# Kernel tuning notes

Measured on AMD Instinct MI355X. Metric: run time of the kernel, lower is better.

Reference implementation:

```python
import jax, jax.numpy as jnp
import numpy as np
import math

K_L = 16
EPS = 1e-5


def _knn_idx(xyt, k):
    # xyt: [B,N,3] -> idx of k nearest (incl. self), ascending distance. [B,N,k]
    sq = jnp.sum(xyt * xyt, axis=-1)                      # [B,N]
    d2 = sq[:, :, None] + sq[:, None, :] - 2.0 * jnp.einsum('bnd,bmd->bnm', xyt, xyt)
    _, idx = jax.lax.top_k(-d2, k)                        # smallest distances first
    return idx


def _gather(x, idx):
    # x: [B,N,D], idx: [B,N,K] -> [B,N,K,D]
    return jax.vmap(lambda p, i: p[i])(x, idx)


def setup_inputs() -> dict:
    key = jax.random.key(0)
    ks = jax.random.split(key, 6)
    B, N, C_in, C = 4, 8192, 64, 64
    xytp = jax.random.normal(ks[0], (B, N, 4), jnp.float32)
    features = jax.random.normal(ks[1], (B, N, C_in), jnp.float32)
    pe_w1 = jax.random.normal(ks[2], (4, C), jnp.float32) * (1.0 / math.sqrt(4))
    pe_b1 = jnp.zeros((C,), jnp.float32)
    pe_w2 = jax.random.normal(ks[3], (C, C), jnp.float32) * (1.0 / math.sqrt(C))
    pe_b2 = jnp.zeros((C,), jnp.float32)
    lt_w = jax.random.normal(ks[4], (C_in, 3 * C), jnp.float32) * (1.0 / math.sqrt(C_in))
    lt_b = jnp.zeros((3 * C,), jnp.float32)
    ln_g = jnp.ones((C,), jnp.float32)
    ln_b = jnp.zeros((C,), jnp.float32)
    return dict(xytp=xytp, features=features, pe_w1=pe_w1, pe_b1=pe_b1,
                pe_w2=pe_w2, pe_b2=pe_b2, lt_w=lt_w, lt_b=lt_b,
                ln_g=ln_g, ln_b=ln_b)


def reference(xytp, features, pe_w1, pe_b1, pe_w2, pe_b2, lt_w, lt_b, ln_g, ln_b):
    C = ln_g.shape[0]
    scale = math.sqrt(C)
    xyt = jax.lax.stop_gradient(xytp[:, :, :3])
    idx = _knn_idx(xyt, K_L)                              # [B,N,K]

    # relative position encoding: MLP(Linear-ReLU-Linear) on xytp deltas
    rel = xytp[:, :, None, :] - _gather(xytp, idx)        # [B,N,K,4]
    delta = jax.nn.relu(rel @ pe_w1 + pe_b1) @ pe_w2 + pe_b2  # [B,N,K,C]

    lt = features @ lt_w + lt_b                           # [B,N,3C]
    varphi, psi, alpha = lt[..., :C], lt[..., C:2 * C], lt[..., 2 * C:]
    psi_g = _gather(psi, idx)                             # [B,N,K,C]
    alpha_g = _gather(alpha, idx)                         # [B,N,K,C]

    pre = varphi[:, :, None, :] - psi_g + delta           # [B,N,K,C]
    mu = jnp.mean(pre, axis=-1, keepdims=True)
    var = jnp.mean((pre - mu) ** 2, axis=-1, keepdims=True)
    ln = (pre - mu) * jax.lax.rsqrt(var + EPS) * ln_g + ln_b

    attn = jax.nn.softmax(ln / scale, axis=2)             # softmax over K
    return jnp.sum(attn * (alpha_g + delta), axis=2)      # [B,N,C]
```

## Files before the change

kernel.cpp:

```cpp
#include <hip/hip_runtime.h>
#include <stdint.h>

#define BATCH 4
#define NPTS 8192
#define KNN_K 16
#define GRID 24
#define NCELL (GRID * GRID * GRID)
#define NCELLP (NCELL + 8)

typedef unsigned long long u64;
typedef unsigned int u32;
typedef unsigned short u16;

#define WS_IDX 0u
#define WS_LT 1048576u
#define WS_CNT 26214400u
#define WS_OFF 26435584u
#define WS_CUR 26656896u
#define WS_SP 26878080u
#define WS_GP 27402368u
#define WS_SIDX 27402496u

__device__ __forceinline__ int cellof(float v, float o, float invs) {
  int c = (int)((v - o) * invs);
  return c < GRID - 1 ? c : GRID - 1;
}

__device__ __forceinline__ u32 f2bf(float v) {
  u32 x = __float_as_uint(v);
  return (x + 0x7FFFu + ((x >> 16) & 1u)) >> 16;
}

typedef _Float16 hv2 __attribute__((ext_vector_type(2)));
union U32H2 { u32 u; hv2 h; };
__device__ __forceinline__ float fdot2u(u32 a, u32 b, float c) {
  U32H2 x, y; x.u = a; y.u = b;
  return __builtin_amdgcn_fdot2(x.h, y.h, c, false);
}
__device__ __forceinline__ u16 f16b(float v) {
  union { _Float16 f; u16 b; } c; c.f = (_Float16)v; return c.b;
}
__device__ __forceinline__ u32 pkf16(float a, float b) {
  return (u32)f16b(a) | ((u32)f16b(b) << 16);
}

__global__ __launch_bounds__(256) void k_bbox1(const float4* __restrict__ xytp,
                                               float* __restrict__ part,
                                               int* __restrict__ cnt) {
  const int blk = blockIdx.x;
  const int b = blk >> 5, sub = blk & 31;
  const int t = threadIdx.x;
#pragma unroll
  for (int i = 0; i < 2; ++i) {
    int v = t + i * 256;
    if (v < 432) cnt[blk * 432 + v] = 0;
  }
  float4 p = xytp[(b << 13) + (sub << 8) + t];
  float mnx = p.x, mny = p.y, mnz = p.z;
  float mxx = p.x, mxy = p.y, mxz = p.z;
#pragma unroll
  for (int d = 1; d < 64; d <<= 1) {
    mnx = fminf(mnx, __shfl_xor(mnx, d)); mny = fminf(mny, __shfl_xor(mny, d));
    mnz = fminf(mnz, __shfl_xor(mnz, d)); mxx = fmaxf(mxx, __shfl_xor(mxx, d));
    mxy = fmaxf(mxy, __shfl_xor(mxy, d)); mxz = fmaxf(mxz, __shfl_xor(mxz, d));
  }
  __shared__ float red[4][6];
  const int lane = t & 63, wv = t >> 6;
  if (lane == 0) {
    red[wv][0] = mnx; red[wv][1] = mny; red[wv][2] = mnz;
    red[wv][3] = mxx; red[wv][4] = mxy; red[wv][5] = mxz;
  }
  __syncthreads();
  if (t == 0) {
    for (int w = 1; w < 4; ++w) {
      red[0][0] = fminf(red[0][0], red[w][0]);
      red[0][1] = fminf(red[0][1], red[w][1]);
      red[0][2] = fminf(red[0][2], red[w][2]);
      red[0][3] = fmaxf(red[0][3], red[w][3]);
      red[0][4] = fmaxf(red[0][4], red[w][4]);
      red[0][5] = fmaxf(red[0][5], red[w][5]);
    }
    float* o = part + blk * 8;
    o[0] = red[0][0]; o[1] = red[0][1]; o[2] = red[0][2];
    o[3] = red[0][3]; o[4] = red[0][4]; o[5] = red[0][5];
  }
}

__global__ __launch_bounds__(64) void k_bbox2(const float* __restrict__ part,
                                              float* __restrict__ gp) {
  const int b = blockIdx.x, t = threadIdx.x;
  const float* pp = part + (b * 32 + (t & 31)) * 8;
  float mnx = pp[0], mny = pp[1], mnz = pp[2];
  float mxx = pp[3], mxy = pp[4], mxz = pp[5];
#pragma unroll
  for (int d = 1; d < 64; d <<= 1) {
    mnx = fminf(mnx, __shfl_xor(mnx, d)); mny = fminf(mny, __shfl_xor(mny, d));
    mnz = fminf(mnz, __shfl_xor(mnz, d)); mxx = fmaxf(mxx, __shfl_xor(mxx, d));
    mxy = fmaxf(mxy, __shfl_xor(mxy, d)); mxz = fmaxf(mxz, __shfl_xor(mxz, d));
  }
  if (t == 0) {
    float rmax = fmaxf(mxx - mnx, fmaxf(mxy - mny, mxz - mnz));
    float s = rmax / (float)GRID;
    float* g = gp + b * 8;
    g[0] = mnx; g[1] = mny; g[2] = mnz;
    g[3] = s; g[4] = 1.0f / s;
  }
}

__global__ __launch_bounds__(256) void k_count(const float4* __restrict__ xytp,
                                               const float* __restrict__ gp,
                                               int* __restrict__ cnt) {
  int i = blockIdx.x * 256 + threadIdx.x;
  int b = i >> 13;
  const float* g = gp + b * 8;
  float4 p = xytp[i];
  int cx = cellof(p.x, g[0], g[4]);
  int cy = cellof(p.y, g[1], g[4]);
  int cz = cellof(p.z, g[2], g[4]);
  atomicAdd(&cnt[b * NCELL + (cz * GRID + cy) * GRID + cx], 1);
}

__global__ __launch_bounds__(1024) void k_scan(const int* __restrict__ cnt,
                                               int* __restrict__ offs,
                                               int* __restrict__ curs) {
  __shared__ int wsum[16];
  const int b = blockIdx.x, t = threadIdx.x;
  const int base = b * NCELL;
  const int base2 = b * NCELLP;
  const int lo = t * 14;
  const int hi = lo + 14 < NCELL ? lo + 14 : NCELL;
  int s = 0;
  for (int c = lo; c < hi; ++c) s += cnt[base + c];
  const int lane = t & 63, wv = t >> 6;
  int v = s;
#pragma unroll
  for (int d = 1; d < 64; d <<= 1) {
    int u = __shfl_up(v, d);
    if (lane >= d) v += u;
  }
  if (lane == 63) wsum[wv] = v;
  __syncthreads();
  if (wv == 0 && lane < 16) {
    int x = wsum[lane];
#pragma unroll
    for (int d = 1; d < 16; d <<= 1) {
      int u = __shfl_up(x, d, 16);
      if (lane >= d) x += u;
    }
    wsum[lane] = x;
  }
  __syncthreads();
  int excl = (wv > 0 ? wsum[wv - 1] : 0) + v - s;
  for (int c = lo; c < hi; ++c) {
    offs[base2 + c] = excl;
    curs[base + c] = excl;
    excl += cnt[base + c];
  }
  if (hi == NCELL) offs[base2 + NCELL] = excl;
}

__global__ __launch_bounds__(256) void k_scatter(const float4* __restrict__ xytp,
                                                 const float* __restrict__ gp,
                                                 int* __restrict__ curs,
                                                 float4* __restrict__ spts,
                                                 u16* __restrict__ sidx) {
  int i = blockIdx.x * 256 + threadIdx.x;
  int b = i >> 13, n = i & 8191;
  const float* g = gp + b * 8;
  float4 p = xytp[i];
  int cx = cellof(p.x, g[0], g[4]);
  int cy = cellof(p.y, g[1], g[4]);
  int cz = cellof(p.z, g[2], g[4]);
  int pos = atomicAdd(&curs[b * NCELL + (cz * GRID + cy) * GRID + cx], 1);
  float sq = fmaf(p.z, p.z, fmaf(p.y, p.y, p.x * p.x));
  spts[(b << 13) + pos] = make_float4(p.x, p.y, p.z, sq);
  sidx[(b << 13) + pos] = (u16)n;
}

__global__ __launch_bounds__(1024) void k_order(const float4* __restrict__ spts,
                                                const int* __restrict__ offs,
                                                const float* __restrict__ gp,
                                                u16* __restrict__ ord) {
  __shared__ int hist[32];
  __shared__ int strt[32];
  const int b = blockIdx.x, t = threadIdx.x;
  if (t < 32) hist[t] = 0;
  __syncthreads();
  const float* g = gp + b * 8;
  const int* ob = offs + b * NCELLP;
  const float4* sp = spts + (b << 13);
  int key[8];
#pragma unroll
  for (int it = 0; it < 8; ++it) {
    const int i = t + it * 1024;
    float4 p = sp[i];
    int cx = cellof(p.x, g[0], g[4]);
    int cy = cellof(p.y, g[1], g[4]);
    int cz = cellof(p.z, g[2], g[4]);
    int c = (cz * GRID + cy) * GRID + cx;
    int cc = ob[c + 1] - ob[c];
    key[it] = cc - 1 < 31 ? cc - 1 : 31;
    atomicAdd(&hist[key[it]], 1);
  }
  __syncthreads();
  if (t == 0) {
    int acc = 0;
    for (int k2 = 0; k2 < 32; ++k2) { strt[k2] = acc; acc += hist[k2]; }
  }
  __syncthreads();
  u16* ob2 = ord + (b << 13);
#pragma unroll
  for (int it = 0; it < 8; ++it) {
    const int i = t + it * 1024;
    int pos = atomicAdd(&strt[key[it]], 1);
    ob2[pos] = (u16)i;
  }
}

#define INSERTC(Af, OI)                                                      \
  {                                                                          \
    float dot = q.x * (Af).x;                                                \
    dot = fmaf(q.y, (Af).y, dot);                                            \
    dot = fmaf(q.z, (Af).z, dot);                                            \
    float d2 = (qsq + (Af).w) - 2.0f * dot;                                  \
    unsigned u = __float_as_uint(d2);                                        \
    u ^= (0x80000000u | (unsigned)((int)u >> 31));                           \
    u64 key = ((u64)u << 32) | (OI);                                         \
    if (key < lst[15]) {                                                     \
      u64 x = key;                                                           \
      _Pragma("unroll") for (int p = 0; p < 16; ++p) {                       \
        bool sw = x < lst[p];                                                \
        u64 a = lst[p];                                                      \
        lst[p] = sw ? x : a;                                                 \
        x = sw ? a : x;                                                      \
      }                                                                      \
    }                                                                        \
  }

#define CSWAP(ia, ib)                                                        \
  {                                                                          \
    u64 ta = c[ia], tb2 = c[ib];                                             \
    bool sw = ta > tb2;                                                      \
    c[ia] = sw ? tb2 : ta;                                                   \
    c[ib] = sw ? ta : tb2;                                                   \
  }

__global__ __launch_bounds__(256) void k_query(const float4* __restrict__ spts,
                                               const u16* __restrict__ sidx,
                                               const int* __restrict__ offs,
                                               const float* __restrict__ gp,
                                               const u16* __restrict__ ord,
                                               u16* __restrict__ oidx) {
  const int lane = threadIdx.x & 63;
  const int l = threadIdx.x & 31;
  const int qid = blockIdx.x * 8 + (threadIdx.x >> 5);
  const int b = qid >> 13;
  const int i = ord[(b << 13) + (qid & 8191)];
  const int tb = lane & 32;
  const float4* __restrict__ sp = spts + (b << 13);
  const u16* __restrict__ sx = sidx + (b << 13);
  const int* __restrict__ ob = offs + b * NCELLP;
  const float* g = gp + b * 8;
  float4 q = sp[i];
  const float qsq = q.w;
  const unsigned orig = sx[i];
  const int cx = cellof(q.x, g[0], g[4]);
  const int cy = cellof(q.y, g[1], g[4]);
  const int cz = cellof(q.z, g[2], g[4]);
  const float s = g[3];
  const float fx = q.x - fmaf((float)cx, s, g[0]);
  const float fy = q.y - fmaf((float)cy, s, g[1]);
  const float fz = q.z - fmaf((float)cz, s, g[2]);
  const float mn = fmaxf(
      0.0f, fminf(fminf(fminf(fx, s - fx), fminf(fy, s - fy)),
                  fminf(fz, s - fz)));

  u64 lst[16];
#pragma unroll
  for (int p = 0; p < 16; ++p) lst[p] = ~0ULL;

  for (int r = 0; r <= GRID; ++r) {
    const int W = 2 * r + 1;
    const int nent = 2 * W * W;
    for (int cb = 0; cb < nent; cb += 32) {
      int ms0 = 0, ms1 = 0;
      const int eid = cb + l;
      if (eid < nent) {
        const int rid = eid >> 1, side = eid & 1;
        const int dz = rid / W - r;
        const int dy = rid % W - r;
        const int z2 = cz + dz, y2 = cy + dy;
        if ((unsigned)z2 < GRID && (unsigned)y2 < GRID) {
          const int rowb = (z2 * GRID + y2) * GRID;
          const bool bdry = (dz == -r) || (dz == r) || (dy == -r) || (dy == r);
          if (bdry) {
            if (side == 0) {
              const int xl = cx - r < 0 ? 0 : cx - r;
              const int xh = cx + r > GRID - 1 ? GRID - 1 : cx + r;
              ms0 = ob[rowb + xl];
              ms1 = ob[rowb + xh + 1];
            }
          } else {
            const int x2 = side ? cx + r : cx - r;
            if ((unsigned)x2 < GRID) {
              ms0 = ob[rowb + x2];
              ms1 = ob[rowb + x2 + 1];
            }
          }
        }
      }
      const int len = ms1 - ms0;
      int pre = len;
#pragma unroll
      for (int d = 1; d < 32; d <<= 1) {
        int u2 = __shfl_up(pre, d);
        if (l >= d) pre += u2;
      }
      const int total = __shfl(pre, tb + 31);
      if (total == 0) continue;
      const int base = ms0 - (pre - len);
      for (int vb = 0; vb < total; vb += 32) {
        const int vidx = vb + l;
        int e = 0;
#pragma unroll
        for (int s2 = 16; s2 >= 1; s2 >>= 1) {
          int pv = __shfl(pre, tb + e + s2 - 1);
          if (pv <= vidx) e += s2;
        }
        const int jb = __shfl(base, tb + e);
        if (vidx < total) {
          const int j = jb + vidx;
          float4 A = sp[j];
          unsigned oi = sx[j];
          INSERTC(A, oi)
        }
      }
    }
    const float rs = fmaf((float)r, s, mn);
    const float T = fmaf(rs, rs, -1e-4f);
    unsigned tu = __float_as_uint(T);
    tu ^= (0x80000000u | (unsigned)((int)tu >> 31));
    int c = 0;
#pragma unroll
    for (int p = 0; p < 16; ++p) c += ((unsigned)(lst[p] >> 32) <= tu) ? 1 : 0;
    c += __shfl_xor(c, 1);
    c += __shfl_xor(c, 2);
    c += __shfl_xor(c, 4);
    c += __shfl_xor(c, 8);
    c += __shfl_xor(c, 16);
    if (c >= 16) break;
  }

#pragma unroll
  for (int mm = 1; mm <= 16; mm <<= 1) {
    u64 c[16];
    const bool keepmin = (l & mm) == 0;
#pragma unroll
    for (int p = 0; p < 16; ++p) {
      u64 o = __shfl_xor(lst[15 - p], mm);
      u64 a = lst[p];
      u64 lo = a < o ? a : o;
      u64 hi = a < o ? o : a;
      c[p] = keepmin ? lo : hi;
    }
    CSWAP(0, 8) CSWAP(1, 9) CSWAP(2, 10) CSWAP(3, 11)
    CSWAP(4, 12) CSWAP(5, 13) CSWAP(6, 14) CSWAP(7, 15)
    CSWAP(0, 4) CSWAP(1, 5) CSWAP(2, 6) CSWAP(3, 7)
    CSWAP(8, 12) CSWAP(9, 13) CSWAP(10, 14) CSWAP(11, 15)
    CSWAP(0, 2) CSWAP(1, 3) CSWAP(4, 6) CSWAP(5, 7)
    CSWAP(8, 10) CSWAP(9, 11) CSWAP(12, 14) CSWAP(13, 15)
    CSWAP(0, 1) CSWAP(2, 3) CSWAP(4, 5) CSWAP(6, 7)
    CSWAP(8, 9) CSWAP(10, 11) CSWAP(12, 13) CSWAP(14, 15)
#pragma unroll
    for (int p = 0; p < 16; ++p) lst[p] = c[p];
  }

  if (l == 0) {
    unsigned pk[8];
#pragma unroll
    for (int k = 0; k < 16; k += 2)
      pk[k >> 1] = (unsigned)(lst[k] & 0xFFFFull) |
                   ((unsigned)(lst[k + 1] & 0xFFFFull) << 16);
    unsigned* od = (unsigned*)(oidx + (((size_t)(b << 13) + orig) << 4));
#pragma unroll
    for (int k = 0; k < 8; ++k) od[k] = pk[k];
  }
}

__global__ __launch_bounds__(256) void k_lt(const float* __restrict__ feat,
                                            const float* __restrict__ ltw,
                                            const float* __restrict__ ltb,
                                            float* __restrict__ lt) {
  __shared__ float sw[64][196];
  __shared__ float sf[32][68];
  const int tid = threadIdx.x;
  const int r0 = blockIdx.x * 32;
#pragma unroll
  for (int i = 0; i < 12; ++i) {
    int v = tid + i * 256;
    float4 w4 = ((const float4*)ltw)[v];
    int row = (v * 4) / 192, col = (v * 4) % 192;
    *(float4*)&sw[row][col] = w4;
  }
#pragma unroll
  for (int i = 0; i < 2; ++i) {
    int v = tid + i * 256;
    int row = v >> 4, c4 = v & 15;
    float4 f4 = ((const float4*)(feat + (size_t)(r0 + row) * 64))[c4];
    *(float4*)&sf[row][c4 * 4] = f4;
  }
  __syncthreads();
  const int r = tid >> 3;
  const int c0 = (tid & 7) * 8;
  float acc[24];
#pragma unroll
  for (int m = 0; m < 8; ++m) {
    acc[m] = ltb[c0 + m];
    acc[8 + m] = ltb[64 + c0 + m];
    acc[16 + m] = ltb[128 + c0 + m];
  }
#pragma unroll 4
  for (int j = 0; j < 64; ++j) {
    float f = sf[r][j];
#pragma unroll
    for (int sec = 0; sec < 3; ++sec) {
      float4 w4a = *(const float4*)&sw[j][sec * 64 + c0];
      float4 w4b = *(const float4*)&sw[j][sec * 64 + c0 + 4];
      acc[sec * 8 + 0] = fmaf(f, w4a.x, acc[sec * 8 + 0]);
      acc[sec * 8 + 1] = fmaf(f, w4a.y, acc[sec * 8 + 1]);
      acc[sec * 8 + 2] = fmaf(f, w4a.z, acc[sec * 8 + 2]);
      acc[sec * 8 + 3] = fmaf(f, w4a.w, acc[sec * 8 + 3]);
      acc[sec * 8 + 4] = fmaf(f, w4b.x, acc[sec * 8 + 4]);
      acc[sec * 8 + 5] = fmaf(f, w4b.y, acc[sec * 8 + 5]);
      acc[sec * 8 + 6] = fmaf(f, w4b.z, acc[sec * 8 + 6]);
      acc[sec * 8 + 7] = fmaf(f, w4b.w, acc[sec * 8 + 7]);
    }
  }
  float* orow = lt + (size_t)(r0 + r) * 128;
  *(float4*)&orow[c0] = make_float4(acc[0], acc[1], acc[2], acc[3]);
  *(float4*)&orow[c0 + 4] = make_float4(acc[4], acc[5], acc[6], acc[7]);
  u32 pk[8];
#pragma unroll
  for (int m = 0; m < 8; ++m)
    pk[m] = f2bf(acc[8 + m]) | (f2bf(acc[16 + m]) << 16);
  u32* prow = (u32*)orow + 64 + c0;
  *(uint4*)&prow[0] = make_uint4(pk[0], pk[1], pk[2], pk[3]);
  *(uint4*)&prow[4] = make_uint4(pk[4], pk[5], pk[6], pk[7]);
}

template <int CTRL>
__device__ __forceinline__ float dpp_add_f(float x) {
  int y = __builtin_amdgcn_update_dpp(0, __float_as_int(x), CTRL, 0xf, 0xf,
                                      true);
  return x + __int_as_float(y);
}
__device__ __forceinline__ float wave_sum64(float x) {
  x = dpp_add_f<0x111>(x);
  x = dpp_add_f<0x112>(x);
  x = dpp_add_f<0x114>(x);
  x = dpp_add_f<0x118>(x);
  x = dpp_add_f<0x142>(x);
  x = dpp_add_f<0x143>(x);
  return __int_as_float(__builtin_amdgcn_readlane(__float_as_int(x), 63));
}

__global__ __launch_bounds__(256) void k_main(
    const float4* __restrict__ xytp, const float* __restrict__ lt,
    const u16* __restrict__ knn, const float* __restrict__ pe_w1,
    const float* __restrict__ pe_b1, const float* __restrict__ pe_w2,
    const float* __restrict__ pe_b2, const float* __restrict__ ln_g,
    const float* __restrict__ ln_b, float* __restrict__ out) {
  __shared__ u16 s_h[4][16][64];
  const int lane = threadIdx.x & 63;
  const int wave = threadIdx.x >> 6;
  const int pid = __builtin_amdgcn_readfirstlane(blockIdx.x * 4 + wave);
  const int b = pid >> 13;
  const int n = pid & 8191;

  float w1c[4];
#pragma unroll
  for (int d = 0; d < 4; ++d) w1c[d] = pe_w1[d * 64 + lane];
  const float b1c = pe_b1[lane];
  u32 w2pk[32];
#pragma unroll
  for (int m2 = 0; m2 < 32; ++m2) {
    float a = pe_w2[(2 * m2) * 64 + lane];
    float bb = pe_w2[(2 * m2 + 1) * 64 + lane];
    w2pk[m2] = pkf16(a, bb);
  }
  const float b2c = pe_b2[lane];
  const float gc = ln_g[lane], bc = ln_b[lane];

  int nb[16];
#pragma unroll
  for (int k = 0; k < 16; ++k) nb[k] = knn[pid * 16 + k];

  const float* __restrict__ ltb = lt + (size_t)(b << 13) * 128;
  const float vc = ltb[(size_t)n * 128 + lane];

  const float4 qv = xytp[(b << 13) + n];
#pragma unroll
  for (int k = 0; k < 16; ++k) {
    float4 g = xytp[(b << 13) + nb[k]];
    float r0 = qv.x - g.x, r1 = qv.y - g.y, r2 = qv.z - g.z, r3 = qv.w - g.w;
    float h = fmaf(r3, w1c[3],
                   fmaf(r2, w1c[2], fmaf(r1, w1c[1], fmaf(r0, w1c[0], b1c))));
    s_h[wave][k][lane] = f16b(fmaxf(h, 0.0f));
  }
  __syncthreads();

  u32 uA = ((const u32*)(ltb + (size_t)nb[0] * 128 + 64))[lane];
  u32 uB = ((const u32*)(ltb + (size_t)nb[1] * 128 + 64))[lane];
  float m = -INFINITY, se = 0.f, oacc = 0.f;
#pragma unroll
  for (int k = 0; k < 16; ++k) {
    const u32 uc = (k & 1) ? uB : uA;
    if (k < 14) {
      const u32* prow = (const u32*)(ltb + (size_t)nb[k + 2] * 128 + 64);
      if (k & 1) uB = prow[lane];
      else       uA = prow[lane];
    }
    const float psi_c = __uint_as_float(uc << 16);
    const float alp_c = __uint_as_float(uc & 0xFFFF0000u);
    float acc = b2c;
    const uint4* hp = (const uint4*)&s_h[wave][k][0];
#pragma unroll
    for (int j4 = 0; j4 < 8; ++j4) {
      uint4 hv = hp[j4];
      acc = fdot2u(hv.x, w2pk[j4 * 4 + 0], acc);
      acc = fdot2u(hv.y, w2pk[j4 * 4 + 1], acc);
      acc = fdot2u(hv.z, w2pk[j4 * 4 + 2], acc);
      acc = fdot2u(hv.w, w2pk[j4 * 4 + 3], acc);
    }
    const float pre = (vc - psi_c) + acc;
    const float apd = alp_c + acc;
    const float sm = wave_sum64(pre);
    const float ssm = wave_sum64(pre * pre);
    const float mu = sm * 0.015625f;
    const float var = fmaf(ssm, 0.015625f, -mu * mu);
    const float inv = rsqrtf(var + 1e-5f);
    const float x = fmaf((pre - mu) * inv, gc, bc) * 0.125f;
    const float mn = fmaxf(m, x);
    const float corr = __expf(m - mn);
    const float e = __expf(x - mn);
    se = fmaf(se, corr, e);
    oacc = fmaf(oacc, corr, e * apd);
    m = mn;
  }
  out[(size_t)pid * 64 + lane] = oacc / se;
}

extern "C" void kernel_launch(void* const* d_in, const int* in_sizes, int n_in,
                              void* d_out, int out_size, void* d_ws,
                              size_t ws_size, hipStream_t stream) {
  const float4* xytp = (const float4*)d_in[0];
  const float* features = (const float*)d_in[1];
  const float* pe_w1 = (const float*)d_in[2];
  const float* pe_b1 = (const float*)d_in[3];
  const float* pe_w2 = (const float*)d_in[4];
  const float* pe_b2 = (const float*)d_in[5];
  const float* lt_w = (const float*)d_in[6];
  const float* lt_b = (const float*)d_in[7];
  const float* ln_g = (const float*)d_in[8];
  const float* ln_b = (const float*)d_in[9];
  float* out = (float*)d_out;

  char* ws = (char*)d_ws;
  u16* idxbuf = (u16*)(ws + WS_IDX);
  float* lt = (float*)(ws + WS_LT);
  int* cnt = (int*)(ws + WS_CNT);
  int* offs = (int*)(ws + WS_OFF);
  int* curs = (int*)(ws + WS_CUR);
  float4* spts = (float4*)(ws + WS_SP);
  float* gp = (float*)(ws + WS_GP);
  u16* sidx = (u16*)(ws + WS_SIDX);
  u16* ordb = (u16*)(ws + WS_CNT);

  k_bbox1<<<128, 256, 0, stream>>>(xytp, (float*)(ws + WS_CUR), cnt);
  k_bbox2<<<BATCH, 64, 0, stream>>>((const float*)(ws + WS_CUR), gp);
  k_count<<<(BATCH * NPTS) / 256, 256, 0, stream>>>(xytp, gp, cnt);
  k_scan<<<BATCH, 1024, 0, stream>>>(cnt, offs, curs);
  k_scatter<<<(BATCH * NPTS) / 256, 256, 0, stream>>>(xytp, gp, curs, spts,
                                                      sidx);
  k_order<<<BATCH, 1024, 0, stream>>>(spts, offs, gp, ordb);
  k_query<<<(BATCH * NPTS) / 8, 256, 0, stream>>>(spts, sidx, offs, gp, ordb,
                                                  idxbuf);
  k_lt<<<(BATCH * NPTS) / 32, 256, 0, stream>>>(features, lt_w, lt_b, lt);
  k_main<<<(BATCH * NPTS) / 4, 256, 0, stream>>>(xytp, lt, idxbuf, pe_w1,
                                                 pe_b1, pe_w2, pe_b2, ln_g,
                                                 ln_b, out);
}
```

Baseline: 351.0 us.

## Fuse feature linear transform into kNN query kernel as extra blocks

The standalone k_lt launch is removed, and its work now runs in extra blocks appended to the k_query grid, so the projection overlaps with the kNN search and one launch is saved. The projection is rewritten to stage weights and features in four 16-row chunks, cutting shared memory from about 58KB to about 15KB. The smaller footprint is meant to keep it from limiting k_query occupancy, since both paths share one kernel's LDS allocation. The cost is extra syncthreads and reloads per chunk, plus a branch that may raise register pressure in the query kernel.

```diff
diff --git a/kernel.cpp b/kernel.cpp
--- a/kernel.cpp
+++ b/kernel.cpp
@@ -20,6 +20,9 @@
 #define WS_SP 26878080u
 #define WS_GP 27402368u
 #define WS_SIDX 27402496u
+
+#define NQBLK ((BATCH * NPTS) / 8)
+#define NLBLK ((BATCH * NPTS) / 32)
 
 __device__ __forceinline__ int cellof(float v, float o, float invs) {
   int c = (int)((v - o) * invs);
@@ -245,15 +248,79 @@
     c[ib] = sw ? ta : tb2;                                                   \
   }
 
-__global__ __launch_bounds__(256) void k_query(const float4* __restrict__ spts,
-                                               const u16* __restrict__ sidx,
-                                               const int* __restrict__ offs,
-                                               const float* __restrict__ gp,
-                                               const u16* __restrict__ ord,
-                                               u16* __restrict__ oidx) {
-  const int lane = threadIdx.x & 63;
-  const int l = threadIdx.x & 31;
-  const int qid = blockIdx.x * 8 + (threadIdx.x >> 5);
+__global__ __launch_bounds__(256) void k_query(
+    const float4* __restrict__ spts, const u16* __restrict__ sidx,
+    const int* __restrict__ offs, const float* __restrict__ gp,
+    const u16* __restrict__ ord, u16* __restrict__ oidx,
+    const float* __restrict__ feat, const float* __restrict__ ltw,
+    const float* __restrict__ ltb, float* __restrict__ lt) {
+  __shared__ float sw_c[16][196];
+  __shared__ float sf_c[32][18];
+  const int tid = threadIdx.x;
+
+  if (blockIdx.x >= NQBLK) {
+    const int r0 = (blockIdx.x - NQBLK) * 32;
+    const int r = tid >> 3;
+    const int c0 = (tid & 7) * 8;
+    float acc[24];
+#pragma unroll
+    for (int m = 0; m < 8; ++m) {
+      acc[m] = ltb[c0 + m];
+      acc[8 + m] = ltb[64 + c0 + m];
+      acc[16 + m] = ltb[128 + c0 + m];
+    }
+    for (int ch = 0; ch < 4; ++ch) {
+#pragma unroll
+      for (int i = 0; i < 3; ++i) {
+        int f = tid + i * 256;
+        int row = f / 48, col4 = f % 48;
+        float4 w4 = ((const float4*)ltw)[(ch * 16 + row) * 48 + col4];
+        *(float4*)&sw_c[row][col4 * 4] = w4;
+      }
+      {
+        int v = tid * 2;
+        int row = v >> 4, jj = v & 15;
+        const float2 f2 =
+            *(const float2*)(feat + (size_t)(r0 + row) * 64 + ch * 16 + jj);
+        sf_c[row][jj] = f2.x;
+        sf_c[row][jj + 1] = f2.y;
+      }
+      __syncthreads();
+#pragma unroll 4
+      for (int jj = 0; jj < 16; ++jj) {
+        float f = sf_c[r][jj];
+#pragma unroll
+        for (int sec = 0; sec < 3; ++sec) {
+          float4 w4a = *(const float4*)&sw_c[jj][sec * 64 + c0];
+          float4 w4b = *(const float4*)&sw_c[jj][sec * 64 + c0 + 4];
+          acc[sec * 8 + 0] = fmaf(f, w4a.x, acc[sec * 8 + 0]);
+          acc[sec * 8 + 1] = fmaf(f, w4a.y, acc[sec * 8 + 1]);
+          acc[sec * 8 + 2] = fmaf(f, w4a.z, acc[sec * 8 + 2]);
+          acc[sec * 8 + 3] = fmaf(f, w4a.w, acc[sec * 8 + 3]);
+          acc[sec * 8 + 4] = fmaf(f, w4b.x, acc[sec * 8 + 4]);
+          acc[sec * 8 + 5] = fmaf(f, w4b.y, acc[sec * 8 + 5]);
+          acc[sec * 8 + 6] = fmaf(f, w4b.z, acc[sec * 8 + 6]);
+          acc[sec * 8 + 7] = fmaf(f, w4b.w, acc[sec * 8 + 7]);
+        }
+      }
+      __syncthreads();
+    }
+    float* orow = lt + (size_t)(r0 + r) * 128;
+    *(float4*)&orow[c0] = make_float4(acc[0], acc[1], acc[2], acc[3]);
+    *(float4*)&orow[c0 + 4] = make_float4(acc[4], acc[5], acc[6], acc[7]);
+    u32 pk[8];
+#pragma unroll
+    for (int m = 0; m < 8; ++m)
+      pk[m] = f2bf(acc[8 + m]) | (f2bf(acc[16 + m]) << 16);
+    u32* prow = (u32*)orow + 64 + c0;
+    *(uint4*)&prow[0] = make_uint4(pk[0], pk[1], pk[2], pk[3]);
+    *(uint4*)&prow[4] = make_uint4(pk[4], pk[5], pk[6], pk[7]);
+    return;
+  }
+
+  const int lane = tid & 63;
+  const int l = tid & 31;
+  const int qid = blockIdx.x * 8 + (tid >> 5);
   const int b = qid >> 13;
   const int i = ord[(b << 13) + (qid & 8191)];
   const int tb = lane & 32;
@@ -387,67 +454,6 @@
   }
 }
 
-__global__ __launch_bounds__(256) void k_lt(const float* __restrict__ feat,
-                                            const float* __restrict__ ltw,
-                                            const float* __restrict__ ltb,
-                                            float* __restrict__ lt) {
-  __shared__ float sw[64][196];
-  __shared__ float sf[32][68];
-  const int tid = threadIdx.x;
-  const int r0 = blockIdx.x * 32;
-#pragma unroll
-  for (int i = 0; i < 12; ++i) {
-    int v = tid + i * 256;
-    float4 w4 = ((const float4*)ltw)[v];
-    int row = (v * 4) / 192, col = (v * 4) % 192;
-    *(float4*)&sw[row][col] = w4;
-  }
-#pragma unroll
-  for (int i = 0; i < 2; ++i) {
-    int v = tid + i * 256;
-    int row = v >> 4, c4 = v & 15;
-    float4 f4 = ((const float4*)(feat + (size_t)(r0 + row) * 64))[c4];
-    *(float4*)&sf[row][c4 * 4] = f4;
-  }
-  __syncthreads();
-  const int r = tid >> 3;
-  const int c0 = (tid & 7) * 8;
-  float acc[24];
-#pragma unroll
-  for (int m = 0; m < 8; ++m) {
-    acc[m] = ltb[c0 + m];
-    acc[8 + m] = ltb[64 + c0 + m];
-    acc[16 + m] = ltb[128 + c0 + m];
-  }
-#pragma unroll 4
-  for (int j = 0; j < 64; ++j) {
-    float f = sf[r][j];
-#pragma unroll
-    for (int sec = 0; sec < 3; ++sec) {
-      float4 w4a = *(const float4*)&sw[j][sec * 64 + c0];
-      float4 w4b = *(const float4*)&sw[j][sec * 64 + c0 + 4];
-      acc[sec * 8 + 0] = fmaf(f, w4a.x, acc[sec * 8 + 0]);
-      acc[sec * 8 + 1] = fmaf(f, w4a.y, acc[sec * 8 + 1]);
-      acc[sec * 8 + 2] = fmaf(f, w4a.z, acc[sec * 8 + 2]);
-      acc[sec * 8 + 3] = fmaf(f, w4a.w, acc[sec * 8 + 3]);
-      acc[sec * 8 + 4] = fmaf(f, w4b.x, acc[sec * 8 + 4]);
-      acc[sec * 8 + 5] = fmaf(f, w4b.y, acc[sec * 8 + 5]);
-      acc[sec * 8 + 6] = fmaf(f, w4b.z, acc[sec * 8 + 6]);
-      acc[sec * 8 + 7] = fmaf(f, w4b.w, acc[sec * 8 + 7]);
-    }
-  }
-  float* orow = lt + (size_t)(r0 + r) * 128;
-  *(float4*)&orow[c0] = make_float4(acc[0], acc[1], acc[2], acc[3]);
-  *(float4*)&orow[c0 + 4] = make_float4(acc[4], acc[5], acc[6], acc[7]);
-  u32 pk[8];
-#pragma unroll
-  for (int m = 0; m < 8; ++m)
-    pk[m] = f2bf(acc[8 + m]) | (f2bf(acc[16 + m]) << 16);
-  u32* prow = (u32*)orow + 64 + c0;
-  *(uint4*)&prow[0] = make_uint4(pk[0], pk[1], pk[2], pk[3]);
-  *(uint4*)&prow[4] = make_uint4(pk[4], pk[5], pk[6], pk[7]);
-}
-
 template <int CTRL>
 __device__ __forceinline__ float dpp_add_f(float x) {
   int y = __builtin_amdgcn_update_dpp(0, __float_as_int(x), CTRL, 0xf, 0xf,
@@ -583,9 +589,9 @@
   k_scatter<<<(BATCH * NPTS) / 256, 256, 0, stream>>>(xytp, gp, curs, spts,
                                                       sidx);
   k_order<<<BATCH, 1024, 0, stream>>>(spts, offs, gp, ordb);
-  k_query<<<(BATCH * NPTS) / 8, 256, 0, stream>>>(spts, sidx, offs, gp, ordb,
-                                                  idxbuf);
-  k_lt<<<(BATCH * NPTS) / 32, 256, 0, stream>>>(features, lt_w, lt_b, lt);
+  k_query<<<NQBLK + NLBLK, 256, 0, stream>>>(spts, sidx, offs, gp, ordb,
+                                             idxbuf, features, lt_w, lt_b,
+                                             lt);
   k_main<<<(BATCH * NPTS) / 4, 256, 0, stream>>>(xytp, lt, idxbuf, pe_w1,
                                                  pe_b1, pe_w2, pe_b2, ln_g,
                                                  ln_b, out);
```

Result: faster. 336.1 us (-4.3%).
